# Kernel tuning notes

Hardware: AMD Instinct MI355X
Metric: run time of the kernel (lower is better)

The kernel has to match this reference:

```python
import jax, jax.numpy as jnp
import numpy as np

L = 16            # table_num (levels)
LOG2T = 14
T = 1 << LOG2T    # entries per table
Z = 512           # z_dim
S = 256           # style_dim
IMG = 256         # img_size
RES_MIN, RES_MAX = 16, 256
HID, OUT = 64, 3  # mlp hidden / out dims
B = 8
FDIM = 2 * L      # retrieved feature dim (2 per level)
PRIME = jnp.uint32(2654435761)  # instant-ngp hash prime
GAIN = 1.4142135623730951       # stylegan lrelu gain sqrt(2)
# geometric level resolutions res_min -> res_max
RES = np.floor(RES_MIN * np.exp(np.arange(L) * np.log(RES_MAX / RES_MIN) / (L - 1))).astype(np.float32)


def _lrelu(x):
    return GAIN * jnp.where(x >= 0, x, 0.2 * x)


def _coords():
    c = (jnp.arange(IMG, dtype=jnp.float32) + 0.5) / IMG
    x, y = jnp.meshgrid(c, c, indexing='ij')
    return jnp.stack((x, y), -1).reshape(-1, 2)  # (N, 2), N = IMG*IMG


def _mod_linear(x, s, aw, ab, w, b):
    # StyleGAN2-style modulated linear with demodulation. x: (B,N,in), s: (B,S)
    style = s @ aw + ab                                   # (B, in)
    demod = jax.lax.rsqrt((style ** 2) @ (w ** 2) + 1e-8)  # (B, out)
    return ((x * style[:, None, :]) @ w) * demod[:, None, :] + b


def _forward(z, mw0, mb0, mw1, mb1, mw2, mb2, base_tables, w_mod, b_mod,
             a0w, a0b, w0, bb0, a1w, a1b, w1, bb1, a2w, a2b, w2, bb2):
    s = _lrelu(z @ mw0 + mb0)
    s = _lrelu(s @ mw1 + mb1)
    s = _lrelu(s @ mw2 + mb2)                              # (B, S)
    # style-conditioned hash tables: per-level per-channel modulation of base tables
    scale = 1.0 + (s @ w_mod + b_mod).reshape(-1, L, 1, 2)
    tables = base_tables[None] * scale                     # (B, L, T, 2)

    coords = _coords()                                     # (N, 2)
    offs = jnp.array([[0, 0], [1, 0], [0, 1], [1, 1]], dtype=jnp.uint32)
    feats = []
    for l in range(L):
        pos = coords * RES[l]
        p0 = jnp.floor(pos)
        frac = pos - p0                                    # (N, 2)
        p0i = p0.astype(jnp.uint32)
        cx = p0i[None, :, 0] + offs[:, 0:1]                # (4, N)
        cy = p0i[None, :, 1] + offs[:, 1:2]
        idx = ((cx ^ (cy * PRIME)) & jnp.uint32(T - 1)).astype(jnp.int32)  # (4, N)
        wx = jnp.where(offs[:, 0:1] == 1, frac[None, :, 0], 1.0 - frac[None, :, 0])
        wy = jnp.where(offs[:, 1:2] == 1, frac[None, :, 1], 1.0 - frac[None, :, 1])
        wgt = wx * wy                                      # (4, N)
        tl = tables[:, l]                                  # (B, T, 2)
        f = jnp.take(tl, idx.reshape(-1), axis=1).reshape(tl.shape[0], 4, -1, 2)
        feats.append(jnp.einsum('bcnd,cn->bnd', f, wgt))   # bilinear interp
    h = jnp.concatenate(feats, -1)                         # (B, N, 2L)

    # stacked modulated MLP (3 layers), final tanh, then render to image
    h = _lrelu(_mod_linear(h, s, a0w, a0b, w0, bb0))
    h = _lrelu(_mod_linear(h, s, a1w, a1b, w1, bb1))
    h = jnp.tanh(_mod_linear(h, s, a2w, a2b, w2, bb2))     # (B, N, 3)
    return h.reshape(-1, IMG, IMG, OUT).transpose(0, 3, 1, 2)


def setup_inputs() -> dict:
    key = jax.random.key(0)
    ks = jax.random.split(key, 12)
    nrm = lambda k, sh, sc: jax.random.normal(k, sh, jnp.float32) * sc
    inp = {}
    inp['z'] = jax.random.normal(ks[0], (B, Z), jnp.float32)
    inp['mw0'] = nrm(ks[1], (Z, S), 1 / np.sqrt(Z)); inp['mb0'] = jnp.zeros((S,), jnp.float32)
    inp['mw1'] = nrm(ks[2], (S, S), 1 / np.sqrt(S)); inp['mb1'] = jnp.zeros((S,), jnp.float32)
    inp['mw2'] = nrm(ks[3], (S, S), 1 / np.sqrt(S)); inp['mb2'] = jnp.zeros((S,), jnp.float32)
    inp['base_tables'] = nrm(ks[4], (L, T, 2), 0.1)
    inp['w_mod'] = nrm(ks[5], (S, L * 2), 1 / np.sqrt(S)); inp['b_mod'] = jnp.zeros((L * 2,), jnp.float32)
    inp['a0w'] = nrm(ks[6], (S, FDIM), 1 / np.sqrt(S)); inp['a0b'] = jnp.ones((FDIM,), jnp.float32)
    inp['w0'] = nrm(ks[7], (FDIM, HID), 1 / np.sqrt(FDIM)); inp['bb0'] = jnp.zeros((HID,), jnp.float32)
    inp['a1w'] = nrm(ks[8], (S, HID), 1 / np.sqrt(S)); inp['a1b'] = jnp.ones((HID,), jnp.float32)
    inp['w1'] = nrm(ks[9], (HID, HID), 1 / np.sqrt(HID)); inp['bb1'] = jnp.zeros((HID,), jnp.float32)
    inp['a2w'] = nrm(ks[10], (S, HID), 1 / np.sqrt(S)); inp['a2b'] = jnp.ones((HID,), jnp.float32)
    inp['w2'] = nrm(ks[11], (HID, OUT), 1 / np.sqrt(HID)); inp['bb2'] = jnp.zeros((OUT,), jnp.float32)
    return inp


def reference(z, mw0, mb0, mw1, mb1, mw2, mb2, base_tables, w_mod, b_mod,
              a0w, a0b, w0, bb0, a1w, a1b, w1, bb1, a2w, a2b, w2, bb2):
    return _forward(z, mw0, mb0, mw1, mb1, mw2, mb2, base_tables, w_mod, b_mod,
                    a0w, a0b, w0, bb0, a1w, a1b, w1, bb1, a2w, a2b, w2, bb2)
```

## Files before the change

### kernel.cpp

```cpp
#include <hip/hip_runtime.h>
#include <hip/hip_bf16.h>

#define NLVL 16
#define TSZ  16384
#define NB   8

typedef _Float16 h8 __attribute__((ext_vector_type(8)));
typedef float    f4 __attribute__((ext_vector_type(4)));

#define MFMA16(A,B,C) __builtin_amdgcn_mfma_f32_16x16x32_f16(A,B,C,0,0,0)
#define GAINF 1.41421356237309515f

__device__ const float RES_TAB[16] = {
  16.f, 19.f, 23.f, 27.f, 33.f, 40.f, 48.f, 58.f,
  70.f, 84.f, 101.f, 122.f, 147.f, 176.f, 212.f, 255.f
};

__device__ __forceinline__ float lrelu(float x) {
  float v = x < 0.0f ? 0.2f * x : x;
  return GAINF * v;
}
__device__ __forceinline__ float act(float x) { return fmaxf(x, 0.2f * x); }

__device__ __forceinline__ float tanh_fast(float x) {
  float t = __builtin_amdgcn_exp2f(x * 2.8853900817779268f);
  return 1.0f - 2.0f * __builtin_amdgcn_rcpf(t + 1.0f);
}

__device__ __forceinline__ unsigned pk(float a, float b) {
  union { decltype(__builtin_amdgcn_cvt_pkrtz(0.f, 0.f)) h; unsigned u; } U;
  U.h = __builtin_amdgcn_cvt_pkrtz(a, b);
  return U.u;
}
__device__ __forceinline__ unsigned pk_rne(float a, float b) {
  union { _Float16 h[2]; unsigned u; } U;
  U.h[0] = (_Float16)a; U.h[1] = (_Float16)b;
  return U.u;
}

__device__ __forceinline__ void hash4(const float* __restrict__ bt,
                                      int n, int l0, float* g8)
{
  const float inv = 1.0f / 256.0f;
  float cx = ((n >> 8) + 0.5f) * inv;
  float cy = ((n & 255) + 0.5f) * inv;
#pragma unroll
  for (int j = 0; j < 4; ++j) {
    float res = RES_TAB[l0 + j];
    float px = cx * res, py = cy * res;
    float fx0 = floorf(px), fy0 = floorf(py);
    float fx = px - fx0, fy = py - fy0;
    unsigned x0 = (unsigned)fx0, y0 = (unsigned)fy0;
    unsigned hy0 = y0 * 2654435761u;
    unsigned hy1 = (y0 + 1u) * 2654435761u;
    unsigned i00 = (x0 ^ hy0) & 16383u;
    unsigned i10 = ((x0 + 1u) ^ hy0) & 16383u;
    unsigned i01 = (x0 ^ hy1) & 16383u;
    unsigned i11 = ((x0 + 1u) ^ hy1) & 16383u;
    const float2* tb = (const float2*)(bt + (size_t)(l0 + j) * (TSZ * 2));
    float2 f00 = tb[i00], f10 = tb[i10], f01 = tb[i01], f11 = tb[i11];
    float wx0 = 1.0f - fx, wy0 = 1.0f - fy;
    float w00 = wx0 * wy0, w10 = fx * wy0, w01 = wx0 * fy, w11 = fx * fy;
    g8[2 * j]     = w00 * f00.x + w10 * f10.x + w01 * f01.x + w11 * f11.x;
    g8[2 * j + 1] = w00 * f00.y + w10 * f10.y + w01 * f01.y + w11 * f11.y;
  }
}
__device__ __forceinline__ void hash_features(const float* __restrict__ bt,
                                              int n, float* g)
{
#pragma unroll
  for (int q = 0; q < 4; ++q) hash4(bt, n, q * 4, g + 8 * q);
}

__device__ __forceinline__ void pf16(const float* __restrict__ p, int nf4,
                                     int s, int t, uint2& sink)
{
  int per = nf4 >> 4;
  const uint4* q = (const uint4*)p + (size_t)s * per;
  for (int e = t; e < per; e += 512) {
    uint4 v = q[e];
    sink.x ^= v.x; sink.y ^= v.w;
  }
}

__device__ __forceinline__ void map_layer(const float* __restrict__ xs_in,
                                          float* __restrict__ out_lds,
                                          const float* __restrict__ W,
                                          const float* __restrict__ bias,
                                          int K, int t,
                                          float* __restrict__ part)
{
  const int j4 = (t & 63) * 4;
  const int ks = t >> 6;
  const int chunk = K >> 3;
  const int kb = ks * chunk;
  f4 a0 = {0,0,0,0}, a1 = {0,0,0,0}, a2 = {0,0,0,0}, a3 = {0,0,0,0};
  for (int k0 = 0; k0 < chunk; k0 += 8) {
    f4 wr[8];
#pragma unroll
    for (int u = 0; u < 8; ++u)
      wr[u] = *(const f4*)&W[(kb + k0 + u) * 256 + j4];
    float xr[8];
#pragma unroll
    for (int u = 0; u < 8; ++u) xr[u] = xs_in[kb + k0 + u];
#pragma unroll
    for (int u = 0; u < 8; u += 4) {
      a0 += xr[u + 0] * wr[u + 0];
      a1 += xr[u + 1] * wr[u + 1];
      a2 += xr[u + 2] * wr[u + 2];
      a3 += xr[u + 3] * wr[u + 3];
    }
  }
  *(f4*)&part[ks * 256 + j4] = (a0 + a1) + (a2 + a3);
  __syncthreads();
  if (t < 256) {
    float v = 0.f;
#pragma unroll
    for (int q = 0; q < 8; ++q) v += part[q * 256 + t];
    out_lds[t] = lrelu(bias[t] + v);
  }
  __syncthreads();
}

__global__ void __launch_bounds__(512) k_pre(
    const float* __restrict__ z,
    const float* __restrict__ mw0, const float* __restrict__ mb0,
    const float* __restrict__ mw1, const float* __restrict__ mb1,
    const float* __restrict__ mw2, const float* __restrict__ mb2,
    const float* __restrict__ bt,
    const float* __restrict__ w_mod, const float* __restrict__ b_mod,
    const float* __restrict__ a0w, const float* __restrict__ a0b,
    const float* __restrict__ w0,
    const float* __restrict__ a1w, const float* __restrict__ a1b,
    const float* __restrict__ w1,
    const float* __restrict__ a2w, const float* __restrict__ a2b,
    const float* __restrict__ w2,
    _Float16* __restrict__ W0h, _Float16* __restrict__ W1h,
    _Float16* __restrict__ W2h, _Float16* __restrict__ ghf)
{
  __shared__ __align__(16) unsigned smem[16384];

  const int t = threadIdx.x;

  if (blockIdx.x >= 8) {
    const int hb  = blockIdx.x - 8;
    {
      int s = hb >> 3;
      uint2 sink = {0, 0};
      pf16(mw0,  32768, s, t, sink);
      pf16(mw1,  16384, s, t, sink);
      pf16(mw2,  16384, s, t, sink);
      pf16(w_mod, 2048, s, t, sink);
      pf16(a0w,   2048, s, t, sink);
      pf16(a1w,   4096, s, t, sink);
      pf16(a2w,   4096, s, t, sink);
      pf16(w0,     512, s, t, sink);
      pf16(w1,    1024, s, t, sink);
      asm volatile("" :: "v"(sink.x), "v"(sink.y));
    }

    const int lvl = hb & 15;
    const int pg  = hb >> 4;
    const int gg  = lvl >> 2;
    const int sub = 2 * (lvl & 3);

    const float4* tb4 = (const float4*)(bt + (size_t)lvl * (TSZ * 2));
#pragma unroll
    for (int i = 0; i < 16; ++i) {
      float4 v = tb4[i * 512 + t];
      int e = (i * 512 + t) * 2;
      smem[e]     = pk_rne(v.x, v.y);
      smem[e + 1] = pk_rne(v.z, v.w);
    }
    __syncthreads();

    const int y = t & 255, xsub = t >> 8;
    const float res = RES_TAB[lvl];
    const float inv = 1.0f / 256.0f;
    float cy = (y + 0.5f) * inv;
    float py = cy * res;
    float fy0 = floorf(py);
    float fy = py - fy0;
    unsigned y0 = (unsigned)fy0;
    unsigned hy0 = y0 * 2654435761u;
    unsigned hy1 = (y0 + 1u) * 2654435761u;
    float wy0 = 1.0f - fy;
    const int cc = y & 15, th = y >> 4;

#pragma unroll
    for (int i = 0; i < 16; ++i) {
      int xo = xsub * 16 + i;
      float cx = (pg * 32 + xo + 0.5f) * inv;
      float px = cx * res;
      float fx0 = floorf(px);
      float fx = px - fx0;
      unsigned x0 = (unsigned)fx0;
      unsigned i00 = (x0 ^ hy0) & 16383u;
      unsigned i10 = ((x0 + 1u) ^ hy0) & 16383u;
      unsigned i01 = (x0 ^ hy1) & 16383u;
      unsigned i11 = ((x0 + 1u) ^ hy1) & 16383u;
      union { unsigned u; _Float16 h[2]; } e00, e10, e01, e11;
      e00.u = smem[i00]; e10.u = smem[i10];
      e01.u = smem[i01]; e11.u = smem[i11];
      float wx0 = 1.0f - fx;
      float w00 = wx0 * wy0, w10 = fx * wy0, w01 = wx0 * fy, w11 = fx * fy;
      float gx = w00 * (float)e00.h[0] + w10 * (float)e10.h[0]
               + w01 * (float)e01.h[0] + w11 * (float)e11.h[0];
      float gy = w00 * (float)e00.h[1] + w10 * (float)e10.h[1]
               + w01 * (float)e01.h[1] + w11 * (float)e11.h[1];
      int tile = pg * 512 + xo * 16 + th;
      *(unsigned*)&ghf[(size_t)tile * 512 + (gg * 16 + cc) * 8 + sub] =
          pk_rne(gx, gy);
    }
    return;
  }

  float* F    = (float*)smem;
  float* xs   = F;
  float* sA   = F + 512;
  float* sB   = F + 768;
  float* st0  = F + 1024;
  float* scf  = F + 1056;
  float* st1  = F + 1088;
  float* st2  = F + 1152;
  float* dm0  = F + 1216;
  float* dm1  = F + 1280;
  float* dm2  = F + 1344;
  float* part = F + 2048;

  const int b = blockIdx.x;

  xs[t] = z[b * 512 + t];
  __syncthreads();

  map_layer(xs, sA, mw0, mb0, 512, t, part);
  map_layer(sA, sB, mw1, mb1, 256, t, part);
  map_layer(sB, xs, mw2, mb2, 256, t, part);
  const float* ss = xs;

  {
    const int jg = (t & 7) * 4, kc = t >> 3, kb = kc * 4;
    f4 wmr[4], awr[4];
#pragma unroll
    for (int k = 0; k < 4; ++k) wmr[k] = *(const f4*)&w_mod[(kb + k) * 32 + jg];
#pragma unroll
    for (int k = 0; k < 4; ++k) awr[k] = *(const f4*)&a0w[(kb + k) * 32 + jg];
    f4 am = {0,0,0,0}, as = {0,0,0,0};
#pragma unroll
    for (int k = 0; k < 4; ++k) {
      float sv = ss[kb + k];
      am += sv * wmr[k]; as += sv * awr[k];
    }
    *(f4*)&part[kc * 32 + jg] = am;
    *(f4*)&part[2048 + kc * 32 + jg] = as;
  }
  __syncthreads();
  if (t < 32) {
    float am = b_mod[t], as = a0b[t];
#pragma unroll
    for (int q = 0; q < 64; ++q) { am += part[q * 32 + t]; as += part[2048 + q * 32 + t]; }
    scf[t] = 1.0f + am; st0[t] = as;
  }
  __syncthreads();

  {
    const int jg = (t & 15) * 4, kc = t >> 4, kb = kc * 8;
    f4 w1r[8], w2r[8];
#pragma unroll
    for (int k = 0; k < 8; ++k) w1r[k] = *(const f4*)&a1w[(kb + k) * 64 + jg];
#pragma unroll
    for (int k = 0; k < 8; ++k) w2r[k] = *(const f4*)&a2w[(kb + k) * 64 + jg];
    f4 v1 = {0,0,0,0}, v2 = {0,0,0,0};
#pragma unroll
    for (int k = 0; k < 8; ++k) {
      float sv = ss[kb + k];
      v1 += sv * w1r[k]; v2 += sv * w2r[k];
    }
    *(f4*)&part[kc * 64 + jg] = v1;
    *(f4*)&part[2048 + kc * 64 + jg] = v2;
  }
  __syncthreads();
  if (t >= 128 && t < 192) {
    int j = t - 128;
    float v1 = a1b[j], v2 = a2b[j];
#pragma unroll
    for (int q = 0; q < 32; ++q) { v1 += part[q * 64 + j]; v2 += part[2048 + q * 64 + j]; }
    st1[j] = v1; st2[j] = v2;
  }
  __syncthreads();

  if (t < 256) {
    int j = t & 63, q = t >> 6;
    float wv[8];
#pragma unroll
    for (int i = 0; i < 8; ++i) wv[i] = w0[(q * 8 + i) * 64 + j];
    float acc = (q == 0) ? 1e-8f : 0.f;
#pragma unroll
    for (int i = 0; i < 8; ++i) {
      float p = st0[q * 8 + i] * wv[i]; acc = fmaf(p, p, acc);
    }
    part[t] = acc;
  } else {
    int u = t - 256, j = u & 63, q = u >> 6;
    float wv[16];
#pragma unroll
    for (int k = 0; k < 16; ++k) wv[k] = w1[(q * 16 + k) * 64 + j];
    float acc = (q == 0) ? 1e-8f : 0.f;
#pragma unroll
    for (int k = 0; k < 16; ++k) {
      float p = st1[q * 16 + k] * wv[k]; acc = fmaf(p, p, acc);
    }
    part[256 + u] = acc;
  }
  if (t < 64) {
    int ch = t & 3, q = t >> 2;
    if (ch < 3) {
      float wv[4];
#pragma unroll
      for (int k = 0; k < 4; ++k) wv[k] = w2[(q * 4 + k) * 3 + ch];
      float acc = (q == 0) ? 1e-8f : 0.f;
#pragma unroll
      for (int k = 0; k < 4; ++k) {
        float p = st2[q * 4 + k] * wv[k]; acc = fmaf(p, p, acc);
      }
      part[512 + t] = acc;
    }
  }
  __syncthreads();
  if (t < 64) {
    float a = part[t] + part[64 + t] + part[128 + t] + part[192 + t];
    dm0[t] = 1.0f / sqrtf(a);
  } else if (t < 128) {
    int j = t - 64; float a = 0.f;
#pragma unroll
    for (int q = 0; q < 4; ++q) a += part[256 + q * 64 + j];
    dm1[j] = 1.0f / sqrtf(a);
  } else if (t >= 192 && t < 195) {
    int ch = t - 192; float a = 0.f;
#pragma unroll
    for (int q = 0; q < 16; ++q) a += part[512 + q * 4 + ch];
    dm2[ch] = 1.0f / sqrtf(a);
  }
  __syncthreads();

  for (int f = t; f < 2048; f += 512) {
    int j = f >> 5, i = f & 31;
    W0h[b * 2048 + f] = (_Float16)(scf[i] * st0[i] * w0[i * 64 + j] * dm0[j]);
  }
  for (int f = t; f < 4096; f += 512) {
    int j2 = f >> 6, k = f & 63;
    W1h[b * 4096 + f] = (_Float16)(GAINF * st1[k] * w1[k * 64 + j2] * dm1[j2]);
  }
  for (int f = t; f < 1024; f += 512) {
    int ch = f >> 6, k = f & 63;
    W2h[b * 1024 + f] = (ch < 3) ? (_Float16)(GAINF * st2[k] * w2[k * 3 + ch] * dm2[ch])
                                 : (_Float16)0.0f;
  }
}

__device__ __forceinline__ void st4(_Float16* L, int pix, int jb, f4 v) {
  int ks = jb ^ ((pix & 7) << 3);
  union { unsigned u[2]; uint2 v2; } U;
  U.u[0] = pk(v[0], v[1]); U.u[1] = pk(v[2], v[3]);
  *(uint2*)(L + pix * 64 + ks) = U.v2;
}
__device__ __forceinline__ h8 ldf(const _Float16* L, int pix, int kb) {
  int ks = kb ^ ((pix & 7) << 3);
  return *(const h8*)(L + pix * 64 + ks);
}

template <int FUSED>
__global__ void __launch_bounds__(256) k_mlp(
    const _Float16* __restrict__ W0h, const _Float16* __restrict__ W1h,
    const _Float16* __restrict__ W2h, const _Float16* __restrict__ ghf,
    const float* __restrict__ bt,
    const float* __restrict__ bb0, const float* __restrict__ bb1,
    const float* __restrict__ bb2, float* __restrict__ out)
{
  __shared__ _Float16 lds[4][4096];
  __shared__ _Float16 hb[FUSED ? 8192 : 8];

  const int t = threadIdx.x;
  const int w = t >> 6, lane = t & 63;
  const int c = lane & 15, g = lane >> 4;
  const int b = blockIdx.y;
  const int pixb = blockIdx.x * 256 + w * 64;
  const int tile0 = pixb >> 4;
  _Float16* L = lds[w];

  if constexpr (FUSED) {
    float gl[32];
    hash_features(bt, blockIdx.x * 256 + t, gl);
    int tl = t >> 4, cl = t & 15;
#pragma unroll
    for (int gg = 0; gg < 4; ++gg) {
      union { unsigned u[4]; uint4 v; } U;
      U.u[0] = pk(gl[8 * gg + 0], gl[8 * gg + 1]);
      U.u[1] = pk(gl[8 * gg + 2], gl[8 * gg + 3]);
      U.u[2] = pk(gl[8 * gg + 4], gl[8 * gg + 5]);
      U.u[3] = pk(gl[8 * gg + 6], gl[8 * gg + 7]);
      *(uint4*)&hb[tl * 512 + (gg * 16 + cl) * 8] = U.v;
    }
    __syncthreads();
  }

  h8 A0[4], A1[4][2], A2[2];
#pragma unroll
  for (int jt = 0; jt < 4; ++jt)
    A0[jt] = *(const h8*)&W0h[b * 2048 + (jt * 16 + c) * 32 + 8 * g];
#pragma unroll
  for (int jt = 0; jt < 4; ++jt)
#pragma unroll
    for (int kf = 0; kf < 2; ++kf)
      A1[jt][kf] = *(const h8*)&W1h[b * 4096 + (jt * 16 + c) * 64 + kf * 32 + 8 * g];
#pragma unroll
  for (int kf = 0; kf < 2; ++kf)
    A2[kf] = *(const h8*)&W2h[b * 1024 + c * 64 + kf * 32 + 8 * g];

  f4 bv0[4], bv1[4], bv2;
#pragma unroll
  for (int jt = 0; jt < 4; ++jt) {
    bv0[jt] = *(const f4*)&bb0[jt * 16 + 4 * g];
    bv1[jt] = *(const f4*)&bb1[jt * 16 + 4 * g];
  }
  if (g == 0) { bv2 = f4{bb2[0], bb2[1], bb2[2], 0.0f}; }
  else        { bv2 = f4{0.0f, 0.0f, 0.0f, 0.0f}; }

  f4 acc[4][4];
#pragma unroll
  for (int pt = 0; pt < 4; ++pt) {
    h8 Bh;
    if constexpr (FUSED) {
      Bh = *(const h8*)&hb[(w * 4 + pt) * 512 + lane * 8];
    } else {
      Bh = *(const h8*)&ghf[(size_t)(tile0 + pt) * 512 + lane * 8];
    }
#pragma unroll
    for (int jt = 0; jt < 4; ++jt)
      acc[jt][pt] = MFMA16(A0[jt], Bh, bv0[jt]);
  }

#pragma unroll
  for (int jt = 0; jt < 4; ++jt)
#pragma unroll
    for (int pt = 0; pt < 4; ++pt) {
      f4 v = acc[jt][pt];
#pragma unroll
      for (int r = 0; r < 4; ++r) v[r] = act(v[r]);
      st4(L, pt * 16 + c, jt * 16 + 4 * g, v);
    }

  f4 acc1[4][4];
#pragma unroll
  for (int pt = 0; pt < 4; ++pt) {
    h8 Bf0 = ldf(L, pt * 16 + c, 0 * 32 + 8 * g);
    h8 Bf1 = ldf(L, pt * 16 + c, 1 * 32 + 8 * g);
#pragma unroll
    for (int jt = 0; jt < 4; ++jt) {
      f4 a = MFMA16(A1[jt][0], Bf0, bv1[jt]);
      acc1[jt][pt] = MFMA16(A1[jt][1], Bf1, a);
    }
  }

#pragma unroll
  for (int jt = 0; jt < 4; ++jt)
#pragma unroll
    for (int pt = 0; pt < 4; ++pt) {
      f4 v = acc1[jt][pt];
#pragma unroll
      for (int r = 0; r < 4; ++r) v[r] = act(v[r]);
      st4(L, pt * 16 + c, jt * 16 + 4 * g, v);
    }

#pragma unroll
  for (int pt = 0; pt < 4; ++pt) {
    h8 Bf0 = ldf(L, pt * 16 + c, 0 * 32 + 8 * g);
    h8 Bf1 = ldf(L, pt * 16 + c, 1 * 32 + 8 * g);
    f4 a = MFMA16(A2[0], Bf0, bv2);
    a = MFMA16(A2[1], Bf1, a);
    if (g == 0) {
      int pix = pixb + pt * 16 + c;
#pragma unroll
      for (int r = 0; r < 3; ++r)
        out[((b * 3 + r) << 16) + pix] = tanh_fast(a[r]);
    }
  }
}

extern "C" void kernel_launch(void* const* d_in, const int* in_sizes, int n_in,
                              void* d_out, int out_size, void* d_ws, size_t ws_size,
                              hipStream_t stream)
{
  const float* z    = (const float*)d_in[0];
  const float* mw0  = (const float*)d_in[1];
  const float* mb0  = (const float*)d_in[2];
  const float* mw1  = (const float*)d_in[3];
  const float* mb1  = (const float*)d_in[4];
  const float* mw2  = (const float*)d_in[5];
  const float* mb2  = (const float*)d_in[6];
  const float* bt   = (const float*)d_in[7];
  const float* wmod = (const float*)d_in[8];
  const float* bmod = (const float*)d_in[9];
  const float* a0w  = (const float*)d_in[10];
  const float* a0b  = (const float*)d_in[11];
  const float* w0   = (const float*)d_in[12];
  const float* bb0  = (const float*)d_in[13];
  const float* a1w  = (const float*)d_in[14];
  const float* a1b  = (const float*)d_in[15];
  const float* w1   = (const float*)d_in[16];
  const float* bb1  = (const float*)d_in[17];
  const float* a2w  = (const float*)d_in[18];
  const float* a2b  = (const float*)d_in[19];
  const float* w2   = (const float*)d_in[20];
  const float* bb2  = (const float*)d_in[21];

  char* ws = (char*)d_ws;
  _Float16* W0h = (_Float16*)(ws);
  _Float16* W1h = (_Float16*)(ws + 32768);
  _Float16* W2h = (_Float16*)(ws + 98304);
  _Float16* ghf = (_Float16*)(ws + 114688);
  float* out = (float*)d_out;

  if (ws_size >= (size_t)4308992) {
    k_pre<<<8 + 128, 512, 0, stream>>>(z, mw0, mb0, mw1, mb1, mw2, mb2, bt,
                                       wmod, bmod, a0w, a0b, w0,
                                       a1w, a1b, w1, a2w, a2b, w2,
                                       W0h, W1h, W2h, ghf);
    k_mlp<0><<<dim3(256, NB), 256, 0, stream>>>(W0h, W1h, W2h, ghf, bt,
                                                bb0, bb1, bb2, out);
  } else {
    k_pre<<<8, 512, 0, stream>>>(z, mw0, mb0, mw1, mb1, mw2, mb2, bt,
                                 wmod, bmod, a0w, a0b, w0,
                                 a1w, a1b, w1, a2w, a2b, w2,
                                 W0h, W1h, W2h, ghf);
    k_mlp<1><<<dim3(256, NB), 256, 0, stream>>>(W0h, W1h, W2h, ghf, bt,
                                                bb0, bb1, bb2, out);
  }
}
```

Baseline: 42.28 us.

## Split style mapping MLP across 16 blocks with global atomic barriers

The style-mapping network used to run one batch per block, with each of 8 blocks streaming the full weight matrices. It is now split by input-row slices across 16 blocks. Each block computes partial sums for all 8 batches, writes them to workspace, and synchronizes through a spin-wait atomic counter before reducing. The demodulated weight construction is also distributed across blocks. This cuts the per-block weight traffic and drops the L2 prefetch hack, but adds a memset launch, global barrier latency, and a deadlock risk if not all 16 blocks are co-resident.

```diff
diff --git a/kernel.cpp b/kernel.cpp
--- a/kernel.cpp
+++ b/kernel.cpp
@@ -4,6 +4,7 @@
 #define NLVL 16
 #define TSZ  16384
 #define NB   8
+#define NS   16
 
 typedef _Float16 h8 __attribute__((ext_vector_type(8)));
 typedef float    f4 __attribute__((ext_vector_type(4)));
@@ -72,52 +73,13 @@
   for (int q = 0; q < 4; ++q) hash4(bt, n, q * 4, g + 8 * q);
 }
 
-__device__ __forceinline__ void pf16(const float* __restrict__ p, int nf4,
-                                     int s, int t, uint2& sink)
-{
-  int per = nf4 >> 4;
-  const uint4* q = (const uint4*)p + (size_t)s * per;
-  for (int e = t; e < per; e += 512) {
-    uint4 v = q[e];
-    sink.x ^= v.x; sink.y ^= v.w;
-  }
-}
-
-__device__ __forceinline__ void map_layer(const float* __restrict__ xs_in,
-                                          float* __restrict__ out_lds,
-                                          const float* __restrict__ W,
-                                          const float* __restrict__ bias,
-                                          int K, int t,
-                                          float* __restrict__ part)
-{
-  const int j4 = (t & 63) * 4;
-  const int ks = t >> 6;
-  const int chunk = K >> 3;
-  const int kb = ks * chunk;
-  f4 a0 = {0,0,0,0}, a1 = {0,0,0,0}, a2 = {0,0,0,0}, a3 = {0,0,0,0};
-  for (int k0 = 0; k0 < chunk; k0 += 8) {
-    f4 wr[8];
-#pragma unroll
-    for (int u = 0; u < 8; ++u)
-      wr[u] = *(const f4*)&W[(kb + k0 + u) * 256 + j4];
-    float xr[8];
-#pragma unroll
-    for (int u = 0; u < 8; ++u) xr[u] = xs_in[kb + k0 + u];
-#pragma unroll
-    for (int u = 0; u < 8; u += 4) {
-      a0 += xr[u + 0] * wr[u + 0];
-      a1 += xr[u + 1] * wr[u + 1];
-      a2 += xr[u + 2] * wr[u + 2];
-      a3 += xr[u + 3] * wr[u + 3];
-    }
-  }
-  *(f4*)&part[ks * 256 + j4] = (a0 + a1) + (a2 + a3);
-  __syncthreads();
-  if (t < 256) {
-    float v = 0.f;
-#pragma unroll
-    for (int q = 0; q < 8; ++q) v += part[q * 256 + t];
-    out_lds[t] = lrelu(bias[t] + v);
+__device__ __forceinline__ void gbar(unsigned* cnt, unsigned target) {
+  __syncthreads();
+  if (threadIdx.x == 0) {
+    __threadfence();
+    atomicAdd(cnt, 1u);
+    while (atomicAdd(cnt, 0u) < target) __builtin_amdgcn_s_sleep(8);
+    __threadfence();
   }
   __syncthreads();
 }
@@ -136,29 +98,16 @@
     const float* __restrict__ a2w, const float* __restrict__ a2b,
     const float* __restrict__ w2,
     _Float16* __restrict__ W0h, _Float16* __restrict__ W1h,
-    _Float16* __restrict__ W2h, _Float16* __restrict__ ghf)
+    _Float16* __restrict__ W2h, _Float16* __restrict__ ghf,
+    float* __restrict__ pA, float* __restrict__ pB,
+    float* __restrict__ pP, unsigned* __restrict__ cnt)
 {
   __shared__ __align__(16) unsigned smem[16384];
 
   const int t = threadIdx.x;
 
-  if (blockIdx.x >= 8) {
-    const int hb  = blockIdx.x - 8;
-    {
-      int s = hb >> 3;
-      uint2 sink = {0, 0};
-      pf16(mw0,  32768, s, t, sink);
-      pf16(mw1,  16384, s, t, sink);
-      pf16(mw2,  16384, s, t, sink);
-      pf16(w_mod, 2048, s, t, sink);
-      pf16(a0w,   2048, s, t, sink);
-      pf16(a1w,   4096, s, t, sink);
-      pf16(a2w,   4096, s, t, sink);
-      pf16(w0,     512, s, t, sink);
-      pf16(w1,    1024, s, t, sink);
-      asm volatile("" :: "v"(sink.x), "v"(sink.y));
-    }
-
+  if (blockIdx.x >= NS) {
+    const int hb  = blockIdx.x - NS;
     const int lvl = hb & 15;
     const int pg  = hb >> 4;
     const int gg  = lvl >> 2;
@@ -215,7 +164,269 @@
     return;
   }
 
-  float* F    = (float*)smem;
+  float* F = (float*)smem;
+  float* zsl  = F;
+  float* sAct = F + 256;
+  float* st0  = F + 2304;
+  float* scf  = F + 2560;
+  float* st1  = F + 2816;
+  float* st2  = F + 3328;
+  float* part = F + 4096;
+
+  const int sid = blockIdx.x;
+  const int j = t & 255, rh = t >> 8;
+
+  if (t < 256) zsl[t] = z[(t >> 5) * 512 + sid * 32 + (t & 31)];
+  __syncthreads();
+  {
+    const int r0 = rh * 16;
+    float wv[16];
+#pragma unroll
+    for (int u = 0; u < 16; ++u)
+      wv[u] = mw0[(sid * 32 + r0 + u) * 256 + j];
+    float acc[8] = {0,0,0,0,0,0,0,0};
+#pragma unroll
+    for (int u = 0; u < 16; ++u)
+#pragma unroll
+      for (int b = 0; b < 8; ++b)
+        acc[b] = fmaf(zsl[b * 32 + r0 + u], wv[u], acc[b]);
+#pragma unroll
+    for (int b = 0; b < 8; ++b) part[(rh * 8 + b) * 256 + j] = acc[b];
+  }
+  __syncthreads();
+  if (t < 256)
+#pragma unroll
+    for (int b = 0; b < 8; ++b)
+      pA[(sid * 8 + b) * 256 + t] = part[b * 256 + t] + part[(8 + b) * 256 + t];
+  gbar(cnt, 16);
+
+  {
+    const int bh = t >> 8;
+#pragma unroll
+    for (int bi = 0; bi < 4; ++bi) {
+      int b = bh * 4 + bi;
+      float v = mb0[j];
+#pragma unroll
+      for (int s = 0; s < NS; ++s) v += pA[(s * 8 + b) * 256 + j];
+      sAct[b * 256 + j] = lrelu(v);
+    }
+  }
+  __syncthreads();
+  {
+    const int r0 = sid * 16 + rh * 8;
+    float wv[8];
+#pragma unroll
+    for (int u = 0; u < 8; ++u) wv[u] = mw1[(r0 + u) * 256 + j];
+    float acc[8] = {0,0,0,0,0,0,0,0};
+#pragma unroll
+    for (int u = 0; u < 8; ++u)
+#pragma unroll
+      for (int b = 0; b < 8; ++b)
+        acc[b] = fmaf(sAct[b * 256 + r0 + u], wv[u], acc[b]);
+#pragma unroll
+    for (int b = 0; b < 8; ++b) part[(rh * 8 + b) * 256 + j] = acc[b];
+  }
+  __syncthreads();
+  if (t < 256)
+#pragma unroll
+    for (int b = 0; b < 8; ++b)
+      pB[(sid * 8 + b) * 256 + t] = part[b * 256 + t] + part[(8 + b) * 256 + t];
+  gbar(cnt, 32);
+
+  {
+    const int bh = t >> 8;
+#pragma unroll
+    for (int bi = 0; bi < 4; ++bi) {
+      int b = bh * 4 + bi;
+      float v = mb1[j];
+#pragma unroll
+      for (int s = 0; s < NS; ++s) v += pB[(s * 8 + b) * 256 + j];
+      sAct[b * 256 + j] = lrelu(v);
+    }
+  }
+  __syncthreads();
+  {
+    const int r0 = sid * 16 + rh * 8;
+    float wv[8];
+#pragma unroll
+    for (int u = 0; u < 8; ++u) wv[u] = mw2[(r0 + u) * 256 + j];
+    float acc[8] = {0,0,0,0,0,0,0,0};
+#pragma unroll
+    for (int u = 0; u < 8; ++u)
+#pragma unroll
+      for (int b = 0; b < 8; ++b)
+        acc[b] = fmaf(sAct[b * 256 + r0 + u], wv[u], acc[b]);
+#pragma unroll
+    for (int b = 0; b < 8; ++b) part[(rh * 8 + b) * 256 + j] = acc[b];
+  }
+  __syncthreads();
+  if (t < 256)
+#pragma unroll
+    for (int b = 0; b < 8; ++b)
+      pA[(sid * 8 + b) * 256 + t] = part[b * 256 + t] + part[(8 + b) * 256 + t];
+  gbar(cnt, 48);
+
+  {
+    const int bh = t >> 8;
+#pragma unroll
+    for (int bi = 0; bi < 4; ++bi) {
+      int b = bh * 4 + bi;
+      float v = mb2[j];
+#pragma unroll
+      for (int s = 0; s < NS; ++s) v += pA[(s * 8 + b) * 256 + j];
+      sAct[b * 256 + j] = lrelu(v);
+    }
+  }
+  __syncthreads();
+  if (t < 192) {
+    const int c = t, r0 = sid * 16;
+    float acc[8] = {0,0,0,0,0,0,0,0};
+    for (int u = 0; u < 16; ++u) {
+      int row = r0 + u;
+      float w = (c < 32)  ? w_mod[row * 32 + c]
+              : (c < 64)  ? a0w[row * 32 + (c - 32)]
+              : (c < 128) ? a1w[row * 64 + (c - 64)]
+                          : a2w[row * 64 + (c - 128)];
+#pragma unroll
+      for (int b = 0; b < 8; ++b)
+        acc[b] = fmaf(sAct[b * 256 + row], w, acc[b]);
+    }
+#pragma unroll
+    for (int b = 0; b < 8; ++b) pP[(sid * 8 + b) * 192 + c] = acc[b];
+  }
+  gbar(cnt, 64);
+
+  if (t < 256) {
+    int b = t >> 5, i = t & 31;
+    float am = b_mod[i], as = a0b[i];
+#pragma unroll
+    for (int s = 0; s < NS; ++s) {
+      am += pP[(s * 8 + b) * 192 + i];
+      as += pP[(s * 8 + b) * 192 + 32 + i];
+    }
+    scf[b * 32 + i] = 1.0f + am;
+    st0[b * 32 + i] = as;
+  }
+  {
+    int b = t >> 6, jj = t & 63;
+    float v1 = a1b[jj], v2 = a2b[jj];
+#pragma unroll
+    for (int s = 0; s < NS; ++s) {
+      v1 += pP[(s * 8 + b) * 192 + 64 + jj];
+      v2 += pP[(s * 8 + b) * 192 + 128 + jj];
+    }
+    st1[b * 64 + jj] = v1;
+    st2[b * 64 + jj] = v2;
+  }
+  __syncthreads();
+
+  if (t < 32) {
+    int b = t >> 2, jo = t & 3, jw = sid * 4 + jo;
+    if (jw < 64) {
+      float acc = 1e-8f;
+#pragma unroll
+      for (int i = 0; i < 32; ++i) {
+        float p = st0[b * 32 + i] * w0[i * 64 + jw];
+        acc = fmaf(p, p, acc);
+      }
+      float dm = 1.0f / sqrtf(acc);
+#pragma unroll
+      for (int i = 0; i < 32; ++i)
+        W0h[b * 2048 + jw * 32 + i] =
+            (_Float16)(scf[b * 32 + i] * st0[b * 32 + i] * w0[i * 64 + jw] * dm);
+    }
+  } else if (t >= 64 && t < 96) {
+    int u = t - 64, b = u >> 2, j2 = sid * 4 + (u & 3);
+    if (j2 < 64) {
+      float acc = 1e-8f;
+#pragma unroll
+      for (int k = 0; k < 64; ++k) {
+        float p = st1[b * 64 + k] * w1[k * 64 + j2];
+        acc = fmaf(p, p, acc);
+      }
+      float dm = 1.0f / sqrtf(acc);
+#pragma unroll
+      for (int k = 0; k < 64; ++k)
+        W1h[b * 4096 + j2 * 64 + k] =
+            (_Float16)(GAINF * st1[b * 64 + k] * w1[k * 64 + j2] * dm);
+    }
+  } else if (t >= 128 && t < 136) {
+    int b = t - 128, ch = sid;
+    if (ch < 3) {
+      float acc = 1e-8f;
+#pragma unroll
+      for (int k = 0; k < 64; ++k) {
+        float p = st2[b * 64 + k] * w2[k * 3 + ch];
+        acc = fmaf(p, p, acc);
+      }
+      float dm = 1.0f / sqrtf(acc);
+#pragma unroll
+      for (int k = 0; k < 64; ++k)
+        W2h[b * 1024 + ch * 64 + k] =
+            (_Float16)(GAINF * st2[b * 64 + k] * w2[k * 3 + ch] * dm);
+    } else {
+#pragma unroll
+      for (int k = 0; k < 64; ++k)
+        W2h[b * 1024 + ch * 64 + k] = (_Float16)0.0f;
+    }
+  }
+}
+
+__device__ __forceinline__ void map_layer(const float* __restrict__ xs_in,
+                                          float* __restrict__ out_lds,
+                                          const float* __restrict__ W,
+                                          const float* __restrict__ bias,
+                                          int K, int t,
+                                          float* __restrict__ part)
+{
+  const int j4 = (t & 63) * 4;
+  const int ks = t >> 6;
+  const int chunk = K >> 3;
+  const int kb = ks * chunk;
+  f4 a0 = {0,0,0,0}, a1 = {0,0,0,0}, a2 = {0,0,0,0}, a3 = {0,0,0,0};
+  for (int k0 = 0; k0 < chunk; k0 += 8) {
+    f4 wr[8];
+#pragma unroll
+    for (int u = 0; u < 8; ++u)
+      wr[u] = *(const f4*)&W[(kb + k0 + u) * 256 + j4];
+    float xr[8];
+#pragma unroll
+    for (int u = 0; u < 8; ++u) xr[u] = xs_in[kb + k0 + u];
+#pragma unroll
+    for (int u = 0; u < 8; u += 4) {
+      a0 += xr[u + 0] * wr[u + 0];
+      a1 += xr[u + 1] * wr[u + 1];
+      a2 += xr[u + 2] * wr[u + 2];
+      a3 += xr[u + 3] * wr[u + 3];
+    }
+  }
+  *(f4*)&part[ks * 256 + j4] = (a0 + a1) + (a2 + a3);
+  __syncthreads();
+  if (t < 256) {
+    float v = 0.f;
+#pragma unroll
+    for (int q = 0; q < 8; ++q) v += part[q * 256 + t];
+    out_lds[t] = lrelu(bias[t] + v);
+  }
+  __syncthreads();
+}
+
+__global__ void __launch_bounds__(512) k_style1(
+    const float* __restrict__ z,
+    const float* __restrict__ mw0, const float* __restrict__ mb0,
+    const float* __restrict__ mw1, const float* __restrict__ mb1,
+    const float* __restrict__ mw2, const float* __restrict__ mb2,
+    const float* __restrict__ w_mod, const float* __restrict__ b_mod,
+    const float* __restrict__ a0w, const float* __restrict__ a0b,
+    const float* __restrict__ w0,
+    const float* __restrict__ a1w, const float* __restrict__ a1b,
+    const float* __restrict__ w1,
+    const float* __restrict__ a2w, const float* __restrict__ a2b,
+    const float* __restrict__ w2,
+    _Float16* __restrict__ W0h, _Float16* __restrict__ W1h,
+    _Float16* __restrict__ W2h)
+{
+  __shared__ __align__(16) float F[8192];
   float* xs   = F;
   float* sA   = F + 512;
   float* sB   = F + 768;
@@ -227,12 +438,11 @@
   float* dm1  = F + 1280;
   float* dm2  = F + 1344;
   float* part = F + 2048;
-
+  const int t = threadIdx.x;
   const int b = blockIdx.x;
 
   xs[t] = z[b * 512 + t];
   __syncthreads();
-
   map_layer(xs, sA, mw0, mb0, 512, t, part);
   map_layer(sA, sB, mw1, mb1, 256, t, part);
   map_layer(sB, xs, mw2, mb2, 256, t, part);
@@ -240,16 +450,12 @@
 
   {
     const int jg = (t & 7) * 4, kc = t >> 3, kb = kc * 4;
-    f4 wmr[4], awr[4];
-#pragma unroll
-    for (int k = 0; k < 4; ++k) wmr[k] = *(const f4*)&w_mod[(kb + k) * 32 + jg];
-#pragma unroll
-    for (int k = 0; k < 4; ++k) awr[k] = *(const f4*)&a0w[(kb + k) * 32 + jg];
     f4 am = {0,0,0,0}, as = {0,0,0,0};
 #pragma unroll
     for (int k = 0; k < 4; ++k) {
       float sv = ss[kb + k];
-      am += sv * wmr[k]; as += sv * awr[k];
+      am += sv * *(const f4*)&w_mod[(kb + k) * 32 + jg];
+      as += sv * *(const f4*)&a0w[(kb + k) * 32 + jg];
     }
     *(f4*)&part[kc * 32 + jg] = am;
     *(f4*)&part[2048 + kc * 32 + jg] = as;
@@ -262,90 +468,44 @@
     scf[t] = 1.0f + am; st0[t] = as;
   }
   __syncthreads();
-
   {
     const int jg = (t & 15) * 4, kc = t >> 4, kb = kc * 8;
-    f4 w1r[8], w2r[8];
-#pragma unroll
-    for (int k = 0; k < 8; ++k) w1r[k] = *(const f4*)&a1w[(kb + k) * 64 + jg];
-#pragma unroll
-    for (int k = 0; k < 8; ++k) w2r[k] = *(const f4*)&a2w[(kb + k) * 64 + jg];
     f4 v1 = {0,0,0,0}, v2 = {0,0,0,0};
 #pragma unroll
     for (int k = 0; k < 8; ++k) {
       float sv = ss[kb + k];
-      v1 += sv * w1r[k]; v2 += sv * w2r[k];
+      v1 += sv * *(const f4*)&a1w[(kb + k) * 64 + jg];
+      v2 += sv * *(const f4*)&a2w[(kb + k) * 64 + jg];
     }
     *(f4*)&part[kc * 64 + jg] = v1;
     *(f4*)&part[2048 + kc * 64 + jg] = v2;
   }
   __syncthreads();
   if (t >= 128 && t < 192) {
-    int j = t - 128;
-    float v1 = a1b[j], v2 = a2b[j];
-#pragma unroll
-    for (int q = 0; q < 32; ++q) { v1 += part[q * 64 + j]; v2 += part[2048 + q * 64 + j]; }
-    st1[j] = v1; st2[j] = v2;
-  }
-  __syncthreads();
-
-  if (t < 256) {
-    int j = t & 63, q = t >> 6;
-    float wv[8];
-#pragma unroll
-    for (int i = 0; i < 8; ++i) wv[i] = w0[(q * 8 + i) * 64 + j];
-    float acc = (q == 0) ? 1e-8f : 0.f;
-#pragma unroll
-    for (int i = 0; i < 8; ++i) {
-      float p = st0[q * 8 + i] * wv[i]; acc = fmaf(p, p, acc);
-    }
-    part[t] = acc;
-  } else {
-    int u = t - 256, j = u & 63, q = u >> 6;
-    float wv[16];
-#pragma unroll
-    for (int k = 0; k < 16; ++k) wv[k] = w1[(q * 16 + k) * 64 + j];
-    float acc = (q == 0) ? 1e-8f : 0.f;
-#pragma unroll
-    for (int k = 0; k < 16; ++k) {
-      float p = st1[q * 16 + k] * wv[k]; acc = fmaf(p, p, acc);
-    }
-    part[256 + u] = acc;
-  }
+    int jj = t - 128;
+    float v1 = a1b[jj], v2 = a2b[jj];
+#pragma unroll
+    for (int q = 0; q < 32; ++q) { v1 += part[q * 64 + jj]; v2 += part[2048 + q * 64 + jj]; }
+    st1[jj] = v1; st2[jj] = v2;
+  }
+  __syncthreads();
   if (t < 64) {
-    int ch = t & 3, q = t >> 2;
-    if (ch < 3) {
-      float wv[4];
-#pragma unroll
-      for (int k = 0; k < 4; ++k) wv[k] = w2[(q * 4 + k) * 3 + ch];
-      float acc = (q == 0) ? 1e-8f : 0.f;
-#pragma unroll
-      for (int k = 0; k < 4; ++k) {
-        float p = st2[q * 4 + k] * wv[k]; acc = fmaf(p, p, acc);
-      }
-      part[512 + t] = acc;
-    }
-  }
-  __syncthreads();
-  if (t < 64) {
-    float a = part[t] + part[64 + t] + part[128 + t] + part[192 + t];
-    dm0[t] = 1.0f / sqrtf(a);
+    float acc = 1e-8f;
+    for (int i = 0; i < 32; ++i) { float p = st0[i] * w0[i * 64 + t]; acc = fmaf(p, p, acc); }
+    dm0[t] = 1.0f / sqrtf(acc);
   } else if (t < 128) {
-    int j = t - 64; float a = 0.f;
-#pragma unroll
-    for (int q = 0; q < 4; ++q) a += part[256 + q * 64 + j];
-    dm1[j] = 1.0f / sqrtf(a);
+    int jj = t - 64; float acc = 1e-8f;
+    for (int k = 0; k < 64; ++k) { float p = st1[k] * w1[k * 64 + jj]; acc = fmaf(p, p, acc); }
+    dm1[jj] = 1.0f / sqrtf(acc);
   } else if (t >= 192 && t < 195) {
-    int ch = t - 192; float a = 0.f;
-#pragma unroll
-    for (int q = 0; q < 16; ++q) a += part[512 + q * 4 + ch];
-    dm2[ch] = 1.0f / sqrtf(a);
-  }
-  __syncthreads();
-
+    int ch = t - 192; float acc = 1e-8f;
+    for (int k = 0; k < 64; ++k) { float p = st2[k] * w2[k * 3 + ch]; acc = fmaf(p, p, acc); }
+    dm2[ch] = 1.0f / sqrtf(acc);
+  }
+  __syncthreads();
   for (int f = t; f < 2048; f += 512) {
-    int j = f >> 5, i = f & 31;
-    W0h[b * 2048 + f] = (_Float16)(scf[i] * st0[i] * w0[i * 64 + j] * dm0[j]);
+    int jw = f >> 5, i = f & 31;
+    W0h[b * 2048 + f] = (_Float16)(scf[i] * st0[i] * w0[i * 64 + jw] * dm0[jw]);
   }
   for (int f = t; f < 4096; f += 512) {
     int j2 = f >> 6, k = f & 63;
@@ -519,20 +679,25 @@
   _Float16* W1h = (_Float16*)(ws + 32768);
   _Float16* W2h = (_Float16*)(ws + 98304);
   _Float16* ghf = (_Float16*)(ws + 114688);
+  float*    pA  = (float*)(ws + 4308992);
+  float*    pB  = (float*)(ws + 4440064);
+  float*    pP  = (float*)(ws + 4571136);
+  unsigned* cnt = (unsigned*)(ws + 4669440);
   float* out = (float*)d_out;
 
-  if (ws_size >= (size_t)4308992) {
-    k_pre<<<8 + 128, 512, 0, stream>>>(z, mw0, mb0, mw1, mb1, mw2, mb2, bt,
-                                       wmod, bmod, a0w, a0b, w0,
-                                       a1w, a1b, w1, a2w, a2b, w2,
-                                       W0h, W1h, W2h, ghf);
+  if (ws_size >= (size_t)4669448) {
+    hipMemsetAsync(cnt, 0, 8, stream);
+    k_pre<<<NS + 128, 512, 0, stream>>>(z, mw0, mb0, mw1, mb1, mw2, mb2, bt,
+                                        wmod, bmod, a0w, a0b, w0,
+                                        a1w, a1b, w1, a2w, a2b, w2,
+                                        W0h, W1h, W2h, ghf, pA, pB, pP, cnt);
     k_mlp<0><<<dim3(256, NB), 256, 0, stream>>>(W0h, W1h, W2h, ghf, bt,
                                                 bb0, bb1, bb2, out);
   } else {
-    k_pre<<<8, 512, 0, stream>>>(z, mw0, mb0, mw1, mb1, mw2, mb2, bt,
-                                 wmod, bmod, a0w, a0b, w0,
-                                 a1w, a1b, w1, a2w, a2b, w2,
-                                 W0h, W1h, W2h, ghf);
+    k_style1<<<NB, 512, 0, stream>>>(z, mw0, mb0, mw1, mb1, mw2, mb2,
+                                     wmod, bmod, a0w, a0b, w0,
+                                     a1w, a1b, w1, a2w, a2b, w2,
+                                     W0h, W1h, W2h);
     k_mlp<1><<<dim3(256, NB), 256, 0, stream>>>(W0h, W1h, W2h, ghf, bt,
                                                 bb0, bb1, bb2, out);
   }
```

Result: slower. 52.62 us (+24.4%).

## Convert mapping weights to fp16 in helper blocks and spin-wait before style MLP

Applied to the files above, without the earlier changes.

The 128 hash-table helper blocks in k_pre now convert the three mapping-network weight matrices to fp16 in workspace instead of only prefetching them into cache. They signal completion through a global atomic counter. The 8 style blocks spin on that counter and then run the mapping MLP from the half-size fp16 weights with a wider per-thread layout. This trades fewer weight bytes per style block for an inter-block spin wait that assumes all 136 blocks are co-resident, an extra memset launch, and reduced precision in the mapping weights. The fallback path gets a separate k_style1 kernel that keeps the old fp32 code.

```diff
diff --git a/kernel.cpp b/kernel.cpp
--- a/kernel.cpp
+++ b/kernel.cpp
@@ -72,51 +72,55 @@
   for (int q = 0; q < 4; ++q) hash4(bt, n, q * 4, g + 8 * q);
 }
 
-__device__ __forceinline__ void pf16(const float* __restrict__ p, int nf4,
-                                     int s, int t, uint2& sink)
-{
-  int per = nf4 >> 4;
-  const uint4* q = (const uint4*)p + (size_t)s * per;
-  for (int e = t; e < per; e += 512) {
-    uint4 v = q[e];
-    sink.x ^= v.x; sink.y ^= v.w;
-  }
-}
-
-__device__ __forceinline__ void map_layer(const float* __restrict__ xs_in,
-                                          float* __restrict__ out_lds,
-                                          const float* __restrict__ W,
-                                          const float* __restrict__ bias,
-                                          int K, int t,
-                                          float* __restrict__ part)
-{
-  const int j4 = (t & 63) * 4;
-  const int ks = t >> 6;
-  const int chunk = K >> 3;
+__device__ __forceinline__ void cvt2(const float* __restrict__ src,
+                                     _Float16* __restrict__ dst,
+                                     int n2, int hb, int t)
+{
+  int cnt = n2 >> 7;
+  int base = hb * cnt;
+  for (int k = t; k < cnt; k += 512) {
+    float2 v = ((const float2*)src)[base + k];
+    ((unsigned*)dst)[base + k] = pk_rne(v.x, v.y);
+  }
+}
+
+__device__ __forceinline__ void map_layer_h(const float* __restrict__ xs_in,
+                                            float* __restrict__ out_lds,
+                                            const _Float16* __restrict__ Wh,
+                                            const float* __restrict__ bias,
+                                            int K, int t,
+                                            float* __restrict__ part)
+{
+  const int j8 = (t & 31) * 8;
+  const int ks = t >> 5;
+  const int chunk = K >> 4;
   const int kb = ks * chunk;
-  f4 a0 = {0,0,0,0}, a1 = {0,0,0,0}, a2 = {0,0,0,0}, a3 = {0,0,0,0};
+  f4 acc0 = {0,0,0,0}, acc1 = {0,0,0,0};
   for (int k0 = 0; k0 < chunk; k0 += 8) {
-    f4 wr[8];
+    h8 wr[8];
 #pragma unroll
     for (int u = 0; u < 8; ++u)
-      wr[u] = *(const f4*)&W[(kb + k0 + u) * 256 + j4];
+      wr[u] = *(const h8*)&Wh[(kb + k0 + u) * 256 + j8];
     float xr[8];
 #pragma unroll
     for (int u = 0; u < 8; ++u) xr[u] = xs_in[kb + k0 + u];
 #pragma unroll
-    for (int u = 0; u < 8; u += 4) {
-      a0 += xr[u + 0] * wr[u + 0];
-      a1 += xr[u + 1] * wr[u + 1];
-      a2 += xr[u + 2] * wr[u + 2];
-      a3 += xr[u + 3] * wr[u + 3];
-    }
-  }
-  *(f4*)&part[ks * 256 + j4] = (a0 + a1) + (a2 + a3);
+    for (int u = 0; u < 8; ++u) {
+      float x = xr[u];
+#pragma unroll
+      for (int e = 0; e < 4; ++e) {
+        acc0[e] = fmaf(x, (float)wr[u][e], acc0[e]);
+        acc1[e] = fmaf(x, (float)wr[u][4 + e], acc1[e]);
+      }
+    }
+  }
+  *(f4*)&part[ks * 256 + j8] = acc0;
+  *(f4*)&part[ks * 256 + j8 + 4] = acc1;
   __syncthreads();
   if (t < 256) {
     float v = 0.f;
 #pragma unroll
-    for (int q = 0; q < 8; ++q) v += part[q * 256 + t];
+    for (int q = 0; q < 16; ++q) v += part[q * 256 + t];
     out_lds[t] = lrelu(bias[t] + v);
   }
   __syncthreads();
@@ -136,28 +140,23 @@
     const float* __restrict__ a2w, const float* __restrict__ a2b,
     const float* __restrict__ w2,
     _Float16* __restrict__ W0h, _Float16* __restrict__ W1h,
-    _Float16* __restrict__ W2h, _Float16* __restrict__ ghf)
+    _Float16* __restrict__ W2h, _Float16* __restrict__ ghf,
+    _Float16* __restrict__ wh0, _Float16* __restrict__ wh1,
+    _Float16* __restrict__ wh2, unsigned* __restrict__ cnt)
 {
   __shared__ __align__(16) unsigned smem[16384];
 
   const int t = threadIdx.x;
 
   if (blockIdx.x >= 8) {
-    const int hb  = blockIdx.x - 8;
-    {
-      int s = hb >> 3;
-      uint2 sink = {0, 0};
-      pf16(mw0,  32768, s, t, sink);
-      pf16(mw1,  16384, s, t, sink);
-      pf16(mw2,  16384, s, t, sink);
-      pf16(w_mod, 2048, s, t, sink);
-      pf16(a0w,   2048, s, t, sink);
-      pf16(a1w,   4096, s, t, sink);
-      pf16(a2w,   4096, s, t, sink);
-      pf16(w0,     512, s, t, sink);
-      pf16(w1,    1024, s, t, sink);
-      asm volatile("" :: "v"(sink.x), "v"(sink.y));
-    }
+    const int hb = blockIdx.x - 8;
+
+    cvt2(mw0, wh0, 65536, hb, t);
+    cvt2(mw1, wh1, 32768, hb, t);
+    cvt2(mw2, wh2, 32768, hb, t);
+    __threadfence();
+    __syncthreads();
+    if (t == 0) atomicAdd(cnt, 1u);
 
     const int lvl = hb & 15;
     const int pg  = hb >> 4;
@@ -231,11 +230,16 @@
   const int b = blockIdx.x;
 
   xs[t] = z[b * 512 + t];
-  __syncthreads();
-
-  map_layer(xs, sA, mw0, mb0, 512, t, part);
-  map_layer(sA, sB, mw1, mb1, 256, t, part);
-  map_layer(sB, xs, mw2, mb2, 256, t, part);
+
+  if (t == 0) {
+    while (atomicAdd(cnt, 0u) < 128u) __builtin_amdgcn_s_sleep(8);
+    __threadfence();
+  }
+  __syncthreads();
+
+  map_layer_h(xs, sA, wh0, mb0, 512, t, part);
+  map_layer_h(sA, sB, wh1, mb1, 256, t, part);
+  map_layer_h(sB, xs, wh2, mb2, 256, t, part);
   const float* ss = xs;
 
   {
@@ -346,6 +350,152 @@
   for (int f = t; f < 2048; f += 512) {
     int j = f >> 5, i = f & 31;
     W0h[b * 2048 + f] = (_Float16)(scf[i] * st0[i] * w0[i * 64 + j] * dm0[j]);
+  }
+  for (int f = t; f < 4096; f += 512) {
+    int j2 = f >> 6, k = f & 63;
+    W1h[b * 4096 + f] = (_Float16)(GAINF * st1[k] * w1[k * 64 + j2] * dm1[j2]);
+  }
+  for (int f = t; f < 1024; f += 512) {
+    int ch = f >> 6, k = f & 63;
+    W2h[b * 1024 + f] = (ch < 3) ? (_Float16)(GAINF * st2[k] * w2[k * 3 + ch] * dm2[ch])
+                                 : (_Float16)0.0f;
+  }
+}
+
+__device__ __forceinline__ void map_layer(const float* __restrict__ xs_in,
+                                          float* __restrict__ out_lds,
+                                          const float* __restrict__ W,
+                                          const float* __restrict__ bias,
+                                          int K, int t,
+                                          float* __restrict__ part)
+{
+  const int j4 = (t & 63) * 4;
+  const int ks = t >> 6;
+  const int chunk = K >> 3;
+  const int kb = ks * chunk;
+  f4 a0 = {0,0,0,0}, a1 = {0,0,0,0}, a2 = {0,0,0,0}, a3 = {0,0,0,0};
+  for (int k0 = 0; k0 < chunk; k0 += 8) {
+    f4 wr[8];
+#pragma unroll
+    for (int u = 0; u < 8; ++u)
+      wr[u] = *(const f4*)&W[(kb + k0 + u) * 256 + j4];
+    float xr[8];
+#pragma unroll
+    for (int u = 0; u < 8; ++u) xr[u] = xs_in[kb + k0 + u];
+#pragma unroll
+    for (int u = 0; u < 8; u += 4) {
+      a0 += xr[u + 0] * wr[u + 0];
+      a1 += xr[u + 1] * wr[u + 1];
+      a2 += xr[u + 2] * wr[u + 2];
+      a3 += xr[u + 3] * wr[u + 3];
+    }
+  }
+  *(f4*)&part[ks * 256 + j4] = (a0 + a1) + (a2 + a3);
+  __syncthreads();
+  if (t < 256) {
+    float v = 0.f;
+#pragma unroll
+    for (int q = 0; q < 8; ++q) v += part[q * 256 + t];
+    out_lds[t] = lrelu(bias[t] + v);
+  }
+  __syncthreads();
+}
+
+__global__ void __launch_bounds__(512) k_style1(
+    const float* __restrict__ z,
+    const float* __restrict__ mw0, const float* __restrict__ mb0,
+    const float* __restrict__ mw1, const float* __restrict__ mb1,
+    const float* __restrict__ mw2, const float* __restrict__ mb2,
+    const float* __restrict__ w_mod, const float* __restrict__ b_mod,
+    const float* __restrict__ a0w, const float* __restrict__ a0b,
+    const float* __restrict__ w0,
+    const float* __restrict__ a1w, const float* __restrict__ a1b,
+    const float* __restrict__ w1,
+    const float* __restrict__ a2w, const float* __restrict__ a2b,
+    const float* __restrict__ w2,
+    _Float16* __restrict__ W0h, _Float16* __restrict__ W1h,
+    _Float16* __restrict__ W2h)
+{
+  __shared__ __align__(16) float F[8192];
+  float* xs   = F;
+  float* sA   = F + 512;
+  float* sB   = F + 768;
+  float* st0  = F + 1024;
+  float* scf  = F + 1056;
+  float* st1  = F + 1088;
+  float* st2  = F + 1152;
+  float* dm0  = F + 1216;
+  float* dm1  = F + 1280;
+  float* dm2  = F + 1344;
+  float* part = F + 2048;
+  const int t = threadIdx.x;
+  const int b = blockIdx.x;
+
+  xs[t] = z[b * 512 + t];
+  __syncthreads();
+  map_layer(xs, sA, mw0, mb0, 512, t, part);
+  map_layer(sA, sB, mw1, mb1, 256, t, part);
+  map_layer(sB, xs, mw2, mb2, 256, t, part);
+  const float* ss = xs;
+
+  {
+    const int jg = (t & 7) * 4, kc = t >> 3, kb = kc * 4;
+    f4 am = {0,0,0,0}, as = {0,0,0,0};
+#pragma unroll
+    for (int k = 0; k < 4; ++k) {
+      float sv = ss[kb + k];
+      am += sv * *(const f4*)&w_mod[(kb + k) * 32 + jg];
+      as += sv * *(const f4*)&a0w[(kb + k) * 32 + jg];
+    }
+    *(f4*)&part[kc * 32 + jg] = am;
+    *(f4*)&part[2048 + kc * 32 + jg] = as;
+  }
+  __syncthreads();
+  if (t < 32) {
+    float am = b_mod[t], as = a0b[t];
+#pragma unroll
+    for (int q = 0; q < 64; ++q) { am += part[q * 32 + t]; as += part[2048 + q * 32 + t]; }
+    scf[t] = 1.0f + am; st0[t] = as;
+  }
+  __syncthreads();
+  {
+    const int jg = (t & 15) * 4, kc = t >> 4, kb = kc * 8;
+    f4 v1 = {0,0,0,0}, v2 = {0,0,0,0};
+#pragma unroll
+    for (int k = 0; k < 8; ++k) {
+      float sv = ss[kb + k];
+      v1 += sv * *(const f4*)&a1w[(kb + k) * 64 + jg];
+      v2 += sv * *(const f4*)&a2w[(kb + k) * 64 + jg];
+    }
+    *(f4*)&part[kc * 64 + jg] = v1;
+    *(f4*)&part[2048 + kc * 64 + jg] = v2;
+  }
+  __syncthreads();
+  if (t >= 128 && t < 192) {
+    int jj = t - 128;
+    float v1 = a1b[jj], v2 = a2b[jj];
+#pragma unroll
+    for (int q = 0; q < 32; ++q) { v1 += part[q * 64 + jj]; v2 += part[2048 + q * 64 + jj]; }
+    st1[jj] = v1; st2[jj] = v2;
+  }
+  __syncthreads();
+  if (t < 64) {
+    float acc = 1e-8f;
+    for (int i = 0; i < 32; ++i) { float p = st0[i] * w0[i * 64 + t]; acc = fmaf(p, p, acc); }
+    dm0[t] = 1.0f / sqrtf(acc);
+  } else if (t < 128) {
+    int jj = t - 64; float acc = 1e-8f;
+    for (int k = 0; k < 64; ++k) { float p = st1[k] * w1[k * 64 + jj]; acc = fmaf(p, p, acc); }
+    dm1[jj] = 1.0f / sqrtf(acc);
+  } else if (t >= 192 && t < 195) {
+    int ch = t - 192; float acc = 1e-8f;
+    for (int k = 0; k < 64; ++k) { float p = st2[k] * w2[k * 3 + ch]; acc = fmaf(p, p, acc); }
+    dm2[ch] = 1.0f / sqrtf(acc);
+  }
+  __syncthreads();
+  for (int f = t; f < 2048; f += 512) {
+    int jw = f >> 5, i = f & 31;
+    W0h[b * 2048 + f] = (_Float16)(scf[i] * st0[i] * w0[i * 64 + jw] * dm0[jw]);
   }
   for (int f = t; f < 4096; f += 512) {
     int j2 = f >> 6, k = f & 63;
@@ -519,20 +669,25 @@
   _Float16* W1h = (_Float16*)(ws + 32768);
   _Float16* W2h = (_Float16*)(ws + 98304);
   _Float16* ghf = (_Float16*)(ws + 114688);
+  _Float16* wh0 = (_Float16*)(ws + 4308992);
+  _Float16* wh1 = (_Float16*)(ws + 4571136);
+  _Float16* wh2 = (_Float16*)(ws + 4702208);
+  unsigned* cnt = (unsigned*)(ws + 4833280);
   float* out = (float*)d_out;
 
-  if (ws_size >= (size_t)4308992) {
+  if (ws_size >= (size_t)4833288) {
+    hipMemsetAsync(cnt, 0, 8, stream);
     k_pre<<<8 + 128, 512, 0, stream>>>(z, mw0, mb0, mw1, mb1, mw2, mb2, bt,
                                        wmod, bmod, a0w, a0b, w0,
                                        a1w, a1b, w1, a2w, a2b, w2,
-                                       W0h, W1h, W2h, ghf);
+                                       W0h, W1h, W2h, ghf, wh0, wh1, wh2, cnt);
     k_mlp<0><<<dim3(256, NB), 256, 0, stream>>>(W0h, W1h, W2h, ghf, bt,
                                                 bb0, bb1, bb2, out);
   } else {
-    k_pre<<<8, 512, 0, stream>>>(z, mw0, mb0, mw1, mb1, mw2, mb2, bt,
-                                 wmod, bmod, a0w, a0b, w0,
-                                 a1w, a1b, w1, a2w, a2b, w2,
-                                 W0h, W1h, W2h, ghf);
+    k_style1<<<NB, 512, 0, stream>>>(z, mw0, mb0, mw1, mb1, mw2, mb2,
+                                     wmod, bmod, a0w, a0b, w0,
+                                     a1w, a1b, w1, a2w, a2b, w2,
+                                     W0h, W1h, W2h);
     k_mlp<1><<<dim3(256, NB), 256, 0, stream>>>(W0h, W1h, W2h, ghf, bt,
                                                 bb0, bb1, bb2, out);
   }
```

Result: slower. 67.94 us (+60.7%).
